# Kernel optimization log

Hardware: AMD Instinct MI355X
Metric: run time of the kernel (lower is better)

The kernel has to match this reference:

```python
import jax, jax.numpy as jnp
import numpy as np

N_NODES = 50000
N_EDGES = 500000
F_IN = 16
F_OUT = 16
F_EDGE = 16
HIDDEN = 64


def setup_inputs() -> dict:
    key = jax.random.key(0)
    ks = jax.random.split(key, 9)
    return {
        "x": jax.random.normal(ks[0], (N_NODES, F_IN), dtype=jnp.float32),
        "edge_feat": jax.random.normal(ks[1], (N_EDGES, F_EDGE), dtype=jnp.float32),
        "src": jax.random.randint(ks[2], (N_EDGES,), 0, N_NODES, dtype=jnp.int32),
        "dst": jax.random.randint(ks[3], (N_EDGES,), 0, N_NODES, dtype=jnp.int32),
        "W1": jax.random.normal(ks[4], (F_EDGE, HIDDEN), dtype=jnp.float32) * 0.1,
        "b1": jax.random.normal(ks[5], (HIDDEN,), dtype=jnp.float32) * 0.1,
        "W2": jax.random.normal(ks[6], (HIDDEN, F_IN * F_OUT), dtype=jnp.float32) * 0.1,
        "b2": jax.random.normal(ks[7], (F_IN * F_OUT,), dtype=jnp.float32) * 0.1,
        "bias": jax.random.normal(ks[8], (F_OUT,), dtype=jnp.float32) * 0.1,
    }


def reference(x, edge_feat, src, dst, W1, b1, W2, b2, bias):
    # WeightNet: per-edge MLP producing a [F_IN, F_OUT] weight matrix per edge
    h = jax.nn.relu(edge_feat @ W1 + b1)                 # [E, HIDDEN]
    W = (h @ W2 + b2).reshape(-1, F_IN, F_OUT)           # [E, F_IN, F_OUT]
    # message: bmm(src_h[E,1,in], W[E,in,out]) -> [E, F_OUT]
    msg = jnp.einsum('ei,eio->eo', x[src], W)
    # scatter-mean reduce over destination nodes
    msum = jax.ops.segment_sum(msg, dst, num_segments=N_NODES)
    cnt = jax.ops.segment_sum(jnp.ones((msg.shape[0],), dtype=msg.dtype), dst,
                              num_segments=N_NODES)
    mean = msum / jnp.maximum(cnt, 1.0)[:, None]
    # DGL update_all only updates nodes that receive messages; zero in-degree
    # nodes keep their input 'h' (valid since F_IN == F_OUT)
    out = jnp.where((cnt > 0)[:, None], mean, x)
    return out + bias[None, :]                           # [N, F_OUT]
```

## Files before the change

kernel.cpp:

```cpp
#include <hip/hip_runtime.h>

#define NN 50000
#define NE 500000
#define FIN 16
#define FOUT 16
#define HID 64
#define TROW 1040

typedef unsigned int  uint;
typedef unsigned short ushort;
typedef __fp16 h2 __attribute__((ext_vector_type(2)));

__device__ __forceinline__ ushort f2h(float f) {
    union { __fp16 h; ushort s; } v; v.h = (__fp16)f; return v.s;
}
__device__ __forceinline__ h2 u2h2(uint u) {
    union { uint u; h2 h; } v; v.u = u; return v.h;
}
__device__ __forceinline__ float h2lo(uint u) {
    union { ushort s; __fp16 h; } v; v.s = (ushort)(u & 0xffffu); return (float)v.h;
}
__device__ __forceinline__ float h2hi(uint u) {
    union { ushort s; __fp16 h; } v; v.s = (ushort)(u >> 16); return (float)v.h;
}


__global__ __launch_bounds__(256) void count_w2r(
    const int* __restrict__ src, const int* __restrict__ dst,
    int* __restrict__ deg_s, int* __restrict__ pos_s,
    int* __restrict__ deg_d, int* __restrict__ pos_d,
    const float* __restrict__ W2, const float* __restrict__ b2,
    const float* __restrict__ W1, float* __restrict__ W2R,
    float* __restrict__ W1T)
{
    const int nbc = (NE + 255) / 256;
    if ((int)blockIdx.x < nbc) {
        const int e = blockIdx.x * 256 + threadIdx.x;
        if (e < NE) {
            pos_s[e] = atomicAdd(deg_s + src[e], 1);
            pos_d[e] = atomicAdd(deg_d + dst[e], 1);
        }
    } else {
        const int t = (blockIdx.x - nbc) * 256 + threadIdx.x;
        if (t < 64 * 16) {
            const int j = t >> 4, i = t & 15;
            W1T[t] = W1[i * HID + j];
        }
        if (t < 65 * 256) {
            const int j = t >> 8;
            const int col = t & 255;
            const int i = col >> 4, o = col & 15;
            const float v = (j < 64) ? W2[j * 256 + col] : b2[col];
            W2R[j * 256 + o * 16 + i] = v;
        }
    }
}

__global__ __launch_bounds__(1024) void dgc_scan2(
    const int* __restrict__ degA, int* __restrict__ offA,
    const int* __restrict__ degB, int* __restrict__ offB)
{
    const int* __restrict__ deg = blockIdx.x ? degB : degA;
    int* __restrict__ offs      = blockIdx.x ? offB : offA;
    __shared__ int wsum[16];
    const int tid = threadIdx.x;
    const int lane = tid & 63;
    const int wid = tid >> 6;
    int carry = 0;
    for (int base = 0; base < NN; base += 1024) {
        const int idx = base + tid;
        const int v = (idx < NN) ? deg[idx] : 0;
        int s = v;
        #pragma unroll
        for (int d = 1; d < 64; d <<= 1) {
            int t = __shfl_up(s, d, 64);
            if (lane >= d) s += t;
        }
        if (lane == 63) wsum[wid] = s;
        __syncthreads();
        if (wid == 0 && lane < 16) {
            int w = wsum[lane];
            #pragma unroll
            for (int d = 1; d < 16; d <<= 1) {
                int t = __shfl_up(w, d, 64);
                if (lane >= d) w += t;
            }
            wsum[lane] = w;
        }
        __syncthreads();
        const int wpre = (wid == 0) ? 0 : wsum[wid - 1];
        if (idx < NN) offs[idx] = carry + wpre + (s - v);
        carry += wsum[15];
        __syncthreads();
    }
    if (tid == 0) offs[NN] = carry;
}

__global__ __launch_bounds__(256) void scatter_tprep(
    const int* __restrict__ src, const int* __restrict__ pos_s,
    const int* __restrict__ offs_s, int* __restrict__ eidx_s,
    const float* __restrict__ x, const float* __restrict__ W2R,
    ushort* __restrict__ T)
{
    const int nbs = (NE + 255) / 256;
    if ((int)blockIdx.x < nbs) {
        const int e = blockIdx.x * 256 + threadIdx.x;
        if (e < NE) eidx_s[offs_s[src[e]] + pos_s[e]] = e;
        return;
    }
    const int bid = blockIdx.x - nbs;
    const int tid = threadIdx.x;
    const int jt = tid >> 4, o = tid & 15;
    const int off0 = (jt >> 1) * 32 + o * 2 + (jt & 1);

    float w0[16], w1[16], w2[16], w3[16];
    {
        const float4* p0 = reinterpret_cast<const float4*>(W2R + (jt     ) * 256 + o * 16);
        const float4* p1 = reinterpret_cast<const float4*>(W2R + (jt + 16) * 256 + o * 16);
        const float4* p2 = reinterpret_cast<const float4*>(W2R + (jt + 32) * 256 + o * 16);
        const float4* p3 = reinterpret_cast<const float4*>(W2R + (jt + 48) * 256 + o * 16);
        #pragma unroll
        for (int q = 0; q < 4; ++q) {
            float4 a = p0[q]; w0[4*q]=a.x; w0[4*q+1]=a.y; w0[4*q+2]=a.z; w0[4*q+3]=a.w;
            float4 b = p1[q]; w1[4*q]=b.x; w1[4*q+1]=b.y; w1[4*q+2]=b.z; w1[4*q+3]=b.w;
            float4 c = p2[q]; w2[4*q]=c.x; w2[4*q+1]=c.y; w2[4*q+2]=c.z; w2[4*q+3]=c.w;
            float4 d = p3[q]; w3[4*q]=d.x; w3[4*q+1]=d.y; w3[4*q+2]=d.z; w3[4*q+3]=d.w;
        }
    }
    float wb[16];
    if (jt == 0) {
        const float4* pb = reinterpret_cast<const float4*>(W2R + 64 * 256 + o * 16);
        #pragma unroll
        for (int q = 0; q < 4; ++q) {
            float4 a = pb[q]; wb[4*q]=a.x; wb[4*q+1]=a.y; wb[4*q+2]=a.z; wb[4*q+3]=a.w;
        }
    }

    for (int n = bid; n < NN; n += 2048) {
        float xr[16];
        {
            const float4* p = reinterpret_cast<const float4*>(x) + (size_t)n * 4;
            float4 a = p[0], b = p[1], c = p[2], d = p[3];
            xr[0]=a.x; xr[1]=a.y; xr[2]=a.z;  xr[3]=a.w;
            xr[4]=b.x; xr[5]=b.y; xr[6]=b.z;  xr[7]=b.w;
            xr[8]=c.x; xr[9]=c.y; xr[10]=c.z; xr[11]=c.w;
            xr[12]=d.x; xr[13]=d.y; xr[14]=d.z; xr[15]=d.w;
        }
        ushort* tw = T + (size_t)n * TROW;

        float s0 = xr[0]*w0[0], s1 = xr[0]*w1[0], s2 = xr[0]*w2[0], s3 = xr[0]*w3[0];
        #pragma unroll
        for (int i = 1; i < 16; ++i) {
            s0 = fmaf(xr[i], w0[i], s0);
            s1 = fmaf(xr[i], w1[i], s1);
            s2 = fmaf(xr[i], w2[i], s2);
            s3 = fmaf(xr[i], w3[i], s3);
        }
        tw[off0]       = f2h(s0);
        tw[off0 + 256] = f2h(s1);
        tw[off0 + 512] = f2h(s2);
        tw[off0 + 768] = f2h(s3);
        if (jt == 0) {
            float sb = xr[0]*wb[0];
            #pragma unroll
            for (int i = 1; i < 16; ++i) sb = fmaf(xr[i], wb[i], sb);
            tw[1024 + o] = f2h(sb);
        }
    }
}

__global__ __launch_bounds__(256) void edge_msg6(
    const int* __restrict__ eidx_s, const int* __restrict__ src,
    const int* __restrict__ dst, const float* __restrict__ ef,
    const float* __restrict__ W1T, const float* __restrict__ b1,
    const ushort* __restrict__ T, const int* __restrict__ offs_d,
    const int* __restrict__ pos_d, float* __restrict__ msgbuf)
{
    const int k = blockIdx.x * blockDim.x + threadIdx.x;
    if (k >= NE) return;
    const int e = eidx_s[k];
    const int s = src[e];

    float ea[16];
    {
        const float4* p = reinterpret_cast<const float4*>(ef) + (size_t)e * 4;
        float4 a = p[0], b = p[1], c = p[2], d = p[3];
        ea[0]=a.x; ea[1]=a.y; ea[2]=a.z;  ea[3]=a.w;
        ea[4]=b.x; ea[5]=b.y; ea[6]=b.z;  ea[7]=b.w;
        ea[8]=c.x; ea[9]=c.y; ea[10]=c.z; ea[11]=c.w;
        ea[12]=d.x; ea[13]=d.y; ea[14]=d.z; ea[15]=d.w;
    }

    const ushort* tr = T + (size_t)s * TROW;

    float m0[16];
    {
        uint4 a = *reinterpret_cast<const uint4*>(tr + 1024);
        uint4 b = *reinterpret_cast<const uint4*>(tr + 1032);
        m0[0]=h2lo(a.x);  m0[1]=h2hi(a.x);  m0[2]=h2lo(a.y);  m0[3]=h2hi(a.y);
        m0[4]=h2lo(a.z);  m0[5]=h2hi(a.z);  m0[6]=h2lo(a.w);  m0[7]=h2hi(a.w);
        m0[8]=h2lo(b.x);  m0[9]=h2hi(b.x);  m0[10]=h2lo(b.y); m0[11]=h2hi(b.y);
        m0[12]=h2lo(b.z); m0[13]=h2hi(b.z); m0[14]=h2lo(b.w); m0[15]=h2hi(b.w);
    }

    for (int jp = 0; jp < 32; ++jp) {
        const float* __restrict__ wr = W1T + jp * 32;
        float h0a = b1[2 * jp], h0b = b1[2 * jp + 1];
        #pragma unroll
        for (int i = 0; i < 16; ++i) {
            h0a = fmaf(ea[i], wr[i], h0a);
            h0b = fmaf(ea[i], wr[16 + i], h0b);
        }
        h0a = fmaxf(h0a, 0.f); h0b = fmaxf(h0b, 0.f);
        const h2 hp0 = __builtin_amdgcn_cvt_pkrtz(h0a, h0b);

        const uint4 a0 = *reinterpret_cast<const uint4*>(tr + jp * 32);
        const uint4 b0 = *reinterpret_cast<const uint4*>(tr + jp * 32 + 8);
        const uint4 c0 = *reinterpret_cast<const uint4*>(tr + jp * 32 + 16);
        const uint4 d0 = *reinterpret_cast<const uint4*>(tr + jp * 32 + 24);

        m0[0]  = __builtin_amdgcn_fdot2(hp0, u2h2(a0.x), m0[0],  false);
        m0[1]  = __builtin_amdgcn_fdot2(hp0, u2h2(a0.y), m0[1],  false);
        m0[2]  = __builtin_amdgcn_fdot2(hp0, u2h2(a0.z), m0[2],  false);
        m0[3]  = __builtin_amdgcn_fdot2(hp0, u2h2(a0.w), m0[3],  false);
        m0[4]  = __builtin_amdgcn_fdot2(hp0, u2h2(b0.x), m0[4],  false);
        m0[5]  = __builtin_amdgcn_fdot2(hp0, u2h2(b0.y), m0[5],  false);
        m0[6]  = __builtin_amdgcn_fdot2(hp0, u2h2(b0.z), m0[6],  false);
        m0[7]  = __builtin_amdgcn_fdot2(hp0, u2h2(b0.w), m0[7],  false);
        m0[8]  = __builtin_amdgcn_fdot2(hp0, u2h2(c0.x), m0[8],  false);
        m0[9]  = __builtin_amdgcn_fdot2(hp0, u2h2(c0.y), m0[9],  false);
        m0[10] = __builtin_amdgcn_fdot2(hp0, u2h2(c0.z), m0[10], false);
        m0[11] = __builtin_amdgcn_fdot2(hp0, u2h2(c0.w), m0[11], false);
        m0[12] = __builtin_amdgcn_fdot2(hp0, u2h2(d0.x), m0[12], false);
        m0[13] = __builtin_amdgcn_fdot2(hp0, u2h2(d0.y), m0[13], false);
        m0[14] = __builtin_amdgcn_fdot2(hp0, u2h2(d0.z), m0[14], false);
        m0[15] = __builtin_amdgcn_fdot2(hp0, u2h2(d0.w), m0[15], false);
    }

    const int d = dst[e];
    const int slot = offs_d[d] + pos_d[e];
    float4* mr = reinterpret_cast<float4*>(msgbuf + (size_t)slot * 16);
    mr[0] = make_float4(m0[0], m0[1], m0[2], m0[3]);
    mr[1] = make_float4(m0[4], m0[5], m0[6], m0[7]);
    mr[2] = make_float4(m0[8], m0[9], m0[10], m0[11]);
    mr[3] = make_float4(m0[12], m0[13], m0[14], m0[15]);
}

__global__ __launch_bounds__(256) void gather_mean3(
    const float* __restrict__ msgbuf, const int* __restrict__ offs_d,
    const float* __restrict__ x, const float* __restrict__ bias,
    float* __restrict__ out)
{
    const int t = blockIdx.x * blockDim.x + threadIdx.x;
    if (t >= NN * 4) return;
    const int n = t >> 2;
    const int oq = t & 3;
    const int beg = offs_d[n], end = offs_d[n + 1];
    float4 s = make_float4(0.f, 0.f, 0.f, 0.f);
    for (int k = beg; k < end; ++k) {
        const float4 v = *reinterpret_cast<const float4*>(msgbuf + (size_t)k * 16 + oq * 4);
        s.x += v.x; s.y += v.y; s.z += v.z; s.w += v.w;
    }
    const int d = end - beg;
    float4 r;
    if (d > 0) {
        const float inv = 1.f / (float)d;
        r = make_float4(s.x * inv, s.y * inv, s.z * inv, s.w * inv);
    } else {
        r = *reinterpret_cast<const float4*>(x + (size_t)n * 16 + oq * 4);
    }
    const float4 bv = *reinterpret_cast<const float4*>(bias + oq * 4);
    r.x += bv.x; r.y += bv.y; r.z += bv.z; r.w += bv.w;
    *reinterpret_cast<float4*>(out + (size_t)n * 16 + oq * 4) = r;
}

__global__ __launch_bounds__(1024) void dgc_scan(
    const int* __restrict__ deg, int* __restrict__ offs, int n)
{
    __shared__ int wsum[16];
    const int tid = threadIdx.x;
    const int lane = tid & 63;
    const int wid = tid >> 6;
    int carry = 0;
    for (int base = 0; base < n; base += 1024) {
        const int idx = base + tid;
        const int v = (idx < n) ? deg[idx] : 0;
        int s = v;
        #pragma unroll
        for (int d = 1; d < 64; d <<= 1) {
            int t = __shfl_up(s, d, 64);
            if (lane >= d) s += t;
        }
        if (lane == 63) wsum[wid] = s;
        __syncthreads();
        if (wid == 0 && lane < 16) {
            int w = wsum[lane];
            #pragma unroll
            for (int d = 1; d < 16; d <<= 1) {
                int t = __shfl_up(w, d, 64);
                if (lane >= d) w += t;
            }
            wsum[lane] = w;
        }
        __syncthreads();
        const int wpre = (wid == 0) ? 0 : wsum[wid - 1];
        if (idx < n) offs[idx] = carry + wpre + (s - v);
        carry += wsum[15];
        __syncthreads();
    }
    if (tid == 0) offs[n] = carry;
}

__global__ __launch_bounds__(256) void dgc_edge_csr(
    const float* __restrict__ x, const float* __restrict__ ef,
    const int* __restrict__ src, const int* __restrict__ dst,
    const float* __restrict__ W1, const float* __restrict__ b1,
    const float* __restrict__ W2, const float* __restrict__ b2,
    float* __restrict__ msg, int* __restrict__ pos, int* __restrict__ deg)
{
    const int e = blockIdx.x * blockDim.x + threadIdx.x;
    if (e >= NE) return;
    float efv[16];
    {
        const float4* p = reinterpret_cast<const float4*>(ef) + (size_t)e * 4;
        float4 a = p[0], b = p[1], c = p[2], d = p[3];
        efv[0]=a.x; efv[1]=a.y; efv[2]=a.z;  efv[3]=a.w;
        efv[4]=b.x; efv[5]=b.y; efv[6]=b.z;  efv[7]=b.w;
        efv[8]=c.x; efv[9]=c.y; efv[10]=c.z; efv[11]=c.w;
        efv[12]=d.x; efv[13]=d.y; efv[14]=d.z; efv[15]=d.w;
    }
    const int s = src[e];
    float xs[16];
    {
        const float4* p = reinterpret_cast<const float4*>(x) + (size_t)s * 4;
        float4 a = p[0], b = p[1], c = p[2], d = p[3];
        xs[0]=a.x; xs[1]=a.y; xs[2]=a.z;  xs[3]=a.w;
        xs[4]=b.x; xs[5]=b.y; xs[6]=b.z;  xs[7]=b.w;
        xs[8]=c.x; xs[9]=c.y; xs[10]=c.z; xs[11]=c.w;
        xs[12]=d.x; xs[13]=d.y; xs[14]=d.z; xs[15]=d.w;
    }
    float m[16];
    #pragma unroll
    for (int o = 0; o < 16; ++o) m[o] = 0.f;
    #pragma unroll
    for (int i = 0; i < 16; ++i) {
        const float xi = xs[i];
        #pragma unroll
        for (int o = 0; o < 16; ++o) m[o] = fmaf(xi, b2[i * 16 + o], m[o]);
    }
    for (int j = 0; j < HID; ++j) {
        float hj = b1[j];
        #pragma unroll
        for (int i = 0; i < 16; ++i) hj = fmaf(efv[i], W1[i * HID + j], hj);
        hj = fmaxf(hj, 0.f);
        const float* __restrict__ w2r = W2 + (size_t)j * 256;
        float t[16];
        #pragma unroll
        for (int o = 0; o < 16; ++o) t[o] = 0.f;
        #pragma unroll
        for (int i = 0; i < 16; ++i) {
            const float xi = xs[i];
            #pragma unroll
            for (int o = 0; o < 16; ++o) t[o] = fmaf(xi, w2r[i * 16 + o], t[o]);
        }
        #pragma unroll
        for (int o = 0; o < 16; ++o) m[o] = fmaf(hj, t[o], m[o]);
    }
    float4* mr = reinterpret_cast<float4*>(msg + (size_t)e * 16);
    mr[0] = make_float4(m[0], m[1], m[2], m[3]);
    mr[1] = make_float4(m[4], m[5], m[6], m[7]);
    mr[2] = make_float4(m[8], m[9], m[10], m[11]);
    mr[3] = make_float4(m[12], m[13], m[14], m[15]);
    pos[e] = atomicAdd(deg + dst[e], 1);
}

__global__ __launch_bounds__(256) void dgc_scatter(
    const int* __restrict__ dst, const int* __restrict__ pos,
    const int* __restrict__ offs, int* __restrict__ eidx)
{
    const int e = blockIdx.x * blockDim.x + threadIdx.x;
    if (e >= NE) return;
    eidx[offs[dst[e]] + pos[e]] = e;
}

__global__ __launch_bounds__(256) void dgc_gather(
    const float* __restrict__ msg, const int* __restrict__ offs,
    const int* __restrict__ eidx, const float* __restrict__ x,
    const float* __restrict__ bias, float* __restrict__ out)
{
    const int t = blockIdx.x * blockDim.x + threadIdx.x;
    if (t >= NN * FOUT) return;
    const int n = t >> 4;
    const int o = t & 15;
    const int beg = offs[n], end = offs[n + 1];
    float s = 0.f;
    for (int k = beg; k < end; ++k)
        s += msg[(size_t)eidx[k] * 16 + o];
    const int d = end - beg;
    const float v = (d > 0) ? (s / (float)d) : x[t];
    out[t] = v + bias[o];
}

extern "C" void kernel_launch(void* const* d_in, const int* in_sizes, int n_in,
                              void* d_out, int out_size, void* d_ws, size_t ws_size,
                              hipStream_t stream) {
    const float* x    = (const float*)d_in[0];
    const float* ef   = (const float*)d_in[1];
    const int*   src  = (const int*)d_in[2];
    const int*   dst  = (const int*)d_in[3];
    const float* W1   = (const float*)d_in[4];
    const float* b1   = (const float*)d_in[5];
    const float* W2   = (const float*)d_in[6];
    const float* b2   = (const float*)d_in[7];
    const float* bias = (const float*)d_in[8];
    float* out = (float*)d_out;

    ushort* T      = (ushort*)d_ws;
    float*  msgbuf = (float*)(T + (size_t)NN * TROW);
    float*  W2R    = msgbuf + (size_t)NE * 16;
    float*  W1T    = W2R + 65 * 256;
    int*    deg_s  = (int*)(W1T + 64 * 16);
    int*    deg_d  = deg_s + NN;
    int*    offs_s = deg_d + NN;
    int*    offs_d = offs_s + NN + 1;
    int*    pos_s  = offs_d + NN + 1;
    int*    pos_d  = pos_s + NE;
    int*    eidx_s = pos_d + NE;
    const size_t needed =
        (size_t)NN * TROW * 2 +
        ((size_t)NE * 16 + 65 * 256 + 64 * 16) * 4 +
        ((size_t)2 * NN + 2 * (NN + 1) + (size_t)3 * NE) * 4;

    const int nbc = (NE + 255) / 256;

    if (ws_size >= needed) {
        hipMemsetAsync(deg_s, 0, (size_t)2 * NN * sizeof(int), stream);
        count_w2r<<<nbc + 65, 256, 0, stream>>>(
            src, dst, deg_s, pos_s, deg_d, pos_d, W2, b2, W1, W2R, W1T);
        dgc_scan2<<<2, 1024, 0, stream>>>(deg_s, offs_s, deg_d, offs_d);
        scatter_tprep<<<nbc + 2048, 256, 0, stream>>>(
            src, pos_s, offs_s, eidx_s, x, W2R, T);
        edge_msg6<<<nbc, 256, 0, stream>>>(
            eidx_s, src, dst, ef, W1T, b1, T, offs_d, pos_d, msgbuf);
        gather_mean3<<<(NN * 4 + 255) / 256, 256, 0, stream>>>(
            msgbuf, offs_d, x, bias, out);
    } else {
        float* msg  = (float*)d_ws;
        int*   deg  = (int*)(msg + (size_t)NE * 16);
        int*   offs = deg + NN;
        int*   pos  = offs + NN + 1;
        int*   eidx = pos + NE;
        hipMemsetAsync(deg, 0, (size_t)NN * sizeof(int), stream);
        dgc_edge_csr<<<(NE + 255) / 256, 256, 0, stream>>>(
            x, ef, src, dst, W1, b1, W2, b2, msg, pos, deg);
        dgc_scan<<<1, 1024, 0, stream>>>(deg, offs, NN);
        dgc_scatter<<<(NE + 255) / 256, 256, 0, stream>>>(dst, pos, offs, eidx);
        dgc_gather<<<(NN * FOUT + 255) / 256, 256, 0, stream>>>(
            msg, offs, eidx, x, bias, out);
    }
}
```

Measured before the change: 211.7 us.

## Fuse the whole pipeline into one cooperative persistent kernel with grid syncs

```diff
diff --git a/kernel.cpp b/kernel.cpp
--- a/kernel.cpp
+++ b/kernel.cpp
@@ -1,11 +1,13 @@
 #include <hip/hip_runtime.h>
+#include <hip/hip_cooperative_groups.h>
+
+namespace cg = cooperative_groups;
 
 #define NN 50000
 #define NE 500000
-#define FIN 16
-#define FOUT 16
 #define HID 64
 #define TROW 1040
+#define MAXG 2048
 
 typedef unsigned int  uint;
 typedef unsigned short ushort;
@@ -24,6 +26,260 @@
     union { ushort s; __fp16 h; } v; v.s = (ushort)(u >> 16); return (float)v.h;
 }
 
+__device__ void blk_scan_range(const int* __restrict__ deg, int* __restrict__ offs,
+                               int beg, int end, int carry0)
+{
+    __shared__ int wsum[4];
+    __shared__ int wtot;
+    const int tid = threadIdx.x;
+    int carry = carry0;
+    for (int base = beg; base < end; base += 256) {
+        const int idx = base + tid;
+        const bool inb = idx < end;
+        int v = inb ? deg[idx] : 0;
+        int s = v;
+        #pragma unroll
+        for (int d = 1; d < 64; d <<= 1) {
+            int t = __shfl_up(s, d, 64);
+            if ((tid & 63) >= d) s += t;
+        }
+        if ((tid & 63) == 63) wsum[tid >> 6] = s;
+        __syncthreads();
+        if (tid == 0) {
+            int c = 0;
+            #pragma unroll
+            for (int w = 0; w < 4; ++w) { int t = wsum[w]; wsum[w] = c; c += t; }
+            wtot = c;
+        }
+        __syncthreads();
+        if (inb) offs[idx] = carry + wsum[tid >> 6] + (s - v);
+        carry += wtot;
+        __syncthreads();
+    }
+}
+
+struct MegaParams {
+    const float *x, *ef;
+    const int *src, *dst;
+    const float *W1, *b1, *W2, *b2, *bias;
+    float *out;
+    ushort *T;
+    float *msgbuf, *W2R, *W1T;
+    int *deg_s, *deg_d, *offs_s, *offs_d, *pos_s, *pos_d, *eidx_s, *bsum_s, *bsum_d;
+};
+
+__global__ __launch_bounds__(256, 4) void dgc_mega(MegaParams p)
+{
+    cg::grid_group gg = cg::this_grid();
+    const int tid = threadIdx.x;
+    const int bid = blockIdx.x;
+    const int G = gridDim.x;
+    const int gtid = bid * 256 + tid;
+    const int gstride = G * 256;
+
+    for (int i = gtid; i < NN; i += gstride) { p.deg_s[i] = 0; p.deg_d[i] = 0; }
+    gg.sync();
+
+    for (int e = gtid; e < NE; e += gstride) {
+        p.pos_s[e] = atomicAdd(p.deg_s + p.src[e], 1);
+        p.pos_d[e] = atomicAdd(p.deg_d + p.dst[e], 1);
+    }
+    for (int t = gtid; t < 65 * 256; t += gstride) {
+        const int j = t >> 8, col = t & 255;
+        const int i = col >> 4, o = col & 15;
+        const float v = (j < 64) ? p.W2[j * 256 + col] : p.b2[col];
+        p.W2R[j * 256 + o * 16 + i] = v;
+    }
+    for (int t = gtid; t < 64 * 16; t += gstride) {
+        const int j = t >> 4, i = t & 15;
+        p.W1T[t] = p.W1[i * HID + j];
+    }
+    gg.sync();
+
+    const int tile = (NN + G - 1) / G;
+    const int nbeg = bid * tile;
+    const int nend = (nbeg + tile < NN) ? (nbeg + tile) : NN;
+    {
+        int ls = 0, ld = 0;
+        for (int i = nbeg + tid; i < nend; i += 256) { ls += p.deg_s[i]; ld += p.deg_d[i]; }
+        #pragma unroll
+        for (int d = 32; d > 0; d >>= 1) {
+            ls += __shfl_down(ls, d, 64);
+            ld += __shfl_down(ld, d, 64);
+        }
+        __shared__ int reds[4], redd[4];
+        if ((tid & 63) == 0) { reds[tid >> 6] = ls; redd[tid >> 6] = ld; }
+        __syncthreads();
+        if (tid == 0) {
+            p.bsum_s[bid] = reds[0] + reds[1] + reds[2] + reds[3];
+            p.bsum_d[bid] = redd[0] + redd[1] + redd[2] + redd[3];
+        }
+        __syncthreads();
+    }
+    gg.sync();
+    if (bid == 0)      blk_scan_range(p.bsum_s, p.bsum_s, 0, G, 0);
+    else if (bid == 1) blk_scan_range(p.bsum_d, p.bsum_d, 0, G, 0);
+    gg.sync();
+    blk_scan_range(p.deg_s, p.offs_s, nbeg, nend, p.bsum_s[bid]);
+    blk_scan_range(p.deg_d, p.offs_d, nbeg, nend, p.bsum_d[bid]);
+    if (gtid == 0) { p.offs_s[NN] = NE; p.offs_d[NN] = NE; }
+    gg.sync();
+
+    for (int e = gtid; e < NE; e += gstride)
+        p.eidx_s[p.offs_s[p.src[e]] + p.pos_s[e]] = e;
+    {
+        const int jt = tid >> 4, o = tid & 15;
+        const int off0 = (jt >> 1) * 32 + o * 2 + (jt & 1);
+
+        float w0[16], w1[16], w2[16], w3[16];
+        {
+            const float4* p0 = reinterpret_cast<const float4*>(p.W2R + (jt     ) * 256 + o * 16);
+            const float4* p1 = reinterpret_cast<const float4*>(p.W2R + (jt + 16) * 256 + o * 16);
+            const float4* p2 = reinterpret_cast<const float4*>(p.W2R + (jt + 32) * 256 + o * 16);
+            const float4* p3 = reinterpret_cast<const float4*>(p.W2R + (jt + 48) * 256 + o * 16);
+            #pragma unroll
+            for (int q = 0; q < 4; ++q) {
+                float4 a = p0[q]; w0[4*q]=a.x; w0[4*q+1]=a.y; w0[4*q+2]=a.z; w0[4*q+3]=a.w;
+                float4 b = p1[q]; w1[4*q]=b.x; w1[4*q+1]=b.y; w1[4*q+2]=b.z; w1[4*q+3]=b.w;
+                float4 c = p2[q]; w2[4*q]=c.x; w2[4*q+1]=c.y; w2[4*q+2]=c.z; w2[4*q+3]=c.w;
+                float4 d = p3[q]; w3[4*q]=d.x; w3[4*q+1]=d.y; w3[4*q+2]=d.z; w3[4*q+3]=d.w;
+            }
+        }
+        float wb[16];
+        if (jt == 0) {
+            const float4* pb = reinterpret_cast<const float4*>(p.W2R + 64 * 256 + o * 16);
+            #pragma unroll
+            for (int q = 0; q < 4; ++q) {
+                float4 a = pb[q]; wb[4*q]=a.x; wb[4*q+1]=a.y; wb[4*q+2]=a.z; wb[4*q+3]=a.w;
+            }
+        }
+
+        for (int n = bid; n < NN; n += G) {
+            float xr[16];
+            {
+                const float4* q = reinterpret_cast<const float4*>(p.x) + (size_t)n * 4;
+                float4 a = q[0], b = q[1], c = q[2], d = q[3];
+                xr[0]=a.x; xr[1]=a.y; xr[2]=a.z;  xr[3]=a.w;
+                xr[4]=b.x; xr[5]=b.y; xr[6]=b.z;  xr[7]=b.w;
+                xr[8]=c.x; xr[9]=c.y; xr[10]=c.z; xr[11]=c.w;
+                xr[12]=d.x; xr[13]=d.y; xr[14]=d.z; xr[15]=d.w;
+            }
+            ushort* tw = p.T + (size_t)n * TROW;
+
+            float s0 = xr[0]*w0[0], s1 = xr[0]*w1[0], s2 = xr[0]*w2[0], s3 = xr[0]*w3[0];
+            #pragma unroll
+            for (int i = 1; i < 16; ++i) {
+                s0 = fmaf(xr[i], w0[i], s0);
+                s1 = fmaf(xr[i], w1[i], s1);
+                s2 = fmaf(xr[i], w2[i], s2);
+                s3 = fmaf(xr[i], w3[i], s3);
+            }
+            tw[off0]       = f2h(s0);
+            tw[off0 + 256] = f2h(s1);
+            tw[off0 + 512] = f2h(s2);
+            tw[off0 + 768] = f2h(s3);
+            if (jt == 0) {
+                float sb = xr[0]*wb[0];
+                #pragma unroll
+                for (int i = 1; i < 16; ++i) sb = fmaf(xr[i], wb[i], sb);
+                tw[1024 + o] = f2h(sb);
+            }
+        }
+    }
+    gg.sync();
+
+    for (int k = gtid; k < NE; k += gstride) {
+        const int e = p.eidx_s[k];
+        const int s = p.src[e];
+
+        float ea[16];
+        {
+            const float4* q = reinterpret_cast<const float4*>(p.ef) + (size_t)e * 4;
+            float4 a = q[0], b = q[1], c = q[2], d = q[3];
+            ea[0]=a.x; ea[1]=a.y; ea[2]=a.z;  ea[3]=a.w;
+            ea[4]=b.x; ea[5]=b.y; ea[6]=b.z;  ea[7]=b.w;
+            ea[8]=c.x; ea[9]=c.y; ea[10]=c.z; ea[11]=c.w;
+            ea[12]=d.x; ea[13]=d.y; ea[14]=d.z; ea[15]=d.w;
+        }
+
+        const ushort* tr = p.T + (size_t)s * TROW;
+
+        float m0[16];
+        {
+            uint4 a = *reinterpret_cast<const uint4*>(tr + 1024);
+            uint4 b = *reinterpret_cast<const uint4*>(tr + 1032);
+            m0[0]=h2lo(a.x);  m0[1]=h2hi(a.x);  m0[2]=h2lo(a.y);  m0[3]=h2hi(a.y);
+            m0[4]=h2lo(a.z);  m0[5]=h2hi(a.z);  m0[6]=h2lo(a.w);  m0[7]=h2hi(a.w);
+            m0[8]=h2lo(b.x);  m0[9]=h2hi(b.x);  m0[10]=h2lo(b.y); m0[11]=h2hi(b.y);
+            m0[12]=h2lo(b.z); m0[13]=h2hi(b.z); m0[14]=h2lo(b.w); m0[15]=h2hi(b.w);
+        }
+
+        for (int jp = 0; jp < 32; ++jp) {
+            const float* __restrict__ wr = p.W1T + jp * 32;
+            float h0a = p.b1[2 * jp], h0b = p.b1[2 * jp + 1];
+            #pragma unroll
+            for (int i = 0; i < 16; ++i) {
+                h0a = fmaf(ea[i], wr[i], h0a);
+                h0b = fmaf(ea[i], wr[16 + i], h0b);
+            }
+            h0a = fmaxf(h0a, 0.f); h0b = fmaxf(h0b, 0.f);
+            const h2 hp0 = __builtin_amdgcn_cvt_pkrtz(h0a, h0b);
+
+            const uint4 a0 = *reinterpret_cast<const uint4*>(tr + jp * 32);
+            const uint4 b0 = *reinterpret_cast<const uint4*>(tr + jp * 32 + 8);
+            const uint4 c0 = *reinterpret_cast<const uint4*>(tr + jp * 32 + 16);
+            const uint4 d0 = *reinterpret_cast<const uint4*>(tr + jp * 32 + 24);
+
+            m0[0]  = __builtin_amdgcn_fdot2(hp0, u2h2(a0.x), m0[0],  false);
+            m0[1]  = __builtin_amdgcn_fdot2(hp0, u2h2(a0.y), m0[1],  false);
+            m0[2]  = __builtin_amdgcn_fdot2(hp0, u2h2(a0.z), m0[2],  false);
+            m0[3]  = __builtin_amdgcn_fdot2(hp0, u2h2(a0.w), m0[3],  false);
+            m0[4]  = __builtin_amdgcn_fdot2(hp0, u2h2(b0.x), m0[4],  false);
+            m0[5]  = __builtin_amdgcn_fdot2(hp0, u2h2(b0.y), m0[5],  false);
+            m0[6]  = __builtin_amdgcn_fdot2(hp0, u2h2(b0.z), m0[6],  false);
+            m0[7]  = __builtin_amdgcn_fdot2(hp0, u2h2(b0.w), m0[7],  false);
+            m0[8]  = __builtin_amdgcn_fdot2(hp0, u2h2(c0.x), m0[8],  false);
+            m0[9]  = __builtin_amdgcn_fdot2(hp0, u2h2(c0.y), m0[9],  false);
+            m0[10] = __builtin_amdgcn_fdot2(hp0, u2h2(c0.z), m0[10], false);
+            m0[11] = __builtin_amdgcn_fdot2(hp0, u2h2(c0.w), m0[11], false);
+            m0[12] = __builtin_amdgcn_fdot2(hp0, u2h2(d0.x), m0[12], false);
+            m0[13] = __builtin_amdgcn_fdot2(hp0, u2h2(d0.y), m0[13], false);
+            m0[14] = __builtin_amdgcn_fdot2(hp0, u2h2(d0.z), m0[14], false);
+            m0[15] = __builtin_amdgcn_fdot2(hp0, u2h2(d0.w), m0[15], false);
+        }
+
+        const int d = p.dst[e];
+        const int slot = p.offs_d[d] + p.pos_d[e];
+        float4* mr = reinterpret_cast<float4*>(p.msgbuf + (size_t)slot * 16);
+        mr[0] = make_float4(m0[0], m0[1], m0[2], m0[3]);
+        mr[1] = make_float4(m0[4], m0[5], m0[6], m0[7]);
+        mr[2] = make_float4(m0[8], m0[9], m0[10], m0[11]);
+        mr[3] = make_float4(m0[12], m0[13], m0[14], m0[15]);
+    }
+    gg.sync();
+
+    for (int t = gtid; t < NN * 4; t += gstride) {
+        const int n = t >> 2;
+        const int oq = t & 3;
+        const int beg = p.offs_d[n], end = p.offs_d[n + 1];
+        float4 s = make_float4(0.f, 0.f, 0.f, 0.f);
+        for (int k = beg; k < end; ++k) {
+            const float4 v = *reinterpret_cast<const float4*>(p.msgbuf + (size_t)k * 16 + oq * 4);
+            s.x += v.x; s.y += v.y; s.z += v.z; s.w += v.w;
+        }
+        const int d = end - beg;
+        float4 r;
+        if (d > 0) {
+            const float inv = 1.f / (float)d;
+            r = make_float4(s.x * inv, s.y * inv, s.z * inv, s.w * inv);
+        } else {
+            r = *reinterpret_cast<const float4*>(p.x + (size_t)n * 16 + oq * 4);
+        }
+        const float4 bv = *reinterpret_cast<const float4*>(p.bias + oq * 4);
+        r.x += bv.x; r.y += bv.y; r.z += bv.z; r.w += bv.w;
+        *reinterpret_cast<float4*>(p.out + (size_t)n * 16 + oq * 4) = r;
+    }
+}
 
 __global__ __launch_bounds__(256) void count_w2r(
     const int* __restrict__ src, const int* __restrict__ dst,
@@ -139,8 +395,8 @@
     for (int n = bid; n < NN; n += 2048) {
         float xr[16];
         {
-            const float4* p = reinterpret_cast<const float4*>(x) + (size_t)n * 4;
-            float4 a = p[0], b = p[1], c = p[2], d = p[3];
+            const float4* q = reinterpret_cast<const float4*>(x) + (size_t)n * 4;
+            float4 a = q[0], b = q[1], c = q[2], d = q[3];
             xr[0]=a.x; xr[1]=a.y; xr[2]=a.z;  xr[3]=a.w;
             xr[4]=b.x; xr[5]=b.y; xr[6]=b.z;  xr[7]=b.w;
             xr[8]=c.x; xr[9]=c.y; xr[10]=c.z; xr[11]=c.w;
@@ -183,8 +439,8 @@
 
     float ea[16];
     {
-        const float4* p = reinterpret_cast<const float4*>(ef) + (size_t)e * 4;
-        float4 a = p[0], b = p[1], c = p[2], d = p[3];
+        const float4* q = reinterpret_cast<const float4*>(ef) + (size_t)e * 4;
+        float4 a = q[0], b = q[1], c = q[2], d = q[3];
         ea[0]=a.x; ea[1]=a.y; ea[2]=a.z;  ea[3]=a.w;
         ea[4]=b.x; ea[5]=b.y; ea[6]=b.z;  ea[7]=b.w;
         ea[8]=c.x; ea[9]=c.y; ea[10]=c.z; ea[11]=c.w;
@@ -389,7 +645,7 @@
     const float* __restrict__ bias, float* __restrict__ out)
 {
     const int t = blockIdx.x * blockDim.x + threadIdx.x;
-    if (t >= NN * FOUT) return;
+    if (t >= NN * 16) return;
     const int n = t >> 4;
     const int o = t & 15;
     const int beg = offs[n], end = offs[n + 1];
@@ -426,24 +682,47 @@
     int*    pos_s  = offs_d + NN + 1;
     int*    pos_d  = pos_s + NE;
     int*    eidx_s = pos_d + NE;
+    int*    bsum_s = eidx_s + NE;
+    int*    bsum_d = bsum_s + MAXG;
     const size_t needed =
         (size_t)NN * TROW * 2 +
         ((size_t)NE * 16 + 65 * 256 + 64 * 16) * 4 +
-        ((size_t)2 * NN + 2 * (NN + 1) + (size_t)3 * NE) * 4;
+        ((size_t)2 * NN + 2 * (NN + 1) + (size_t)3 * NE + 2 * MAXG) * 4;
 
     const int nbc = (NE + 255) / 256;
 
     if (ws_size >= needed) {
-        hipMemsetAsync(deg_s, 0, (size_t)2 * NN * sizeof(int), stream);
-        count_w2r<<<nbc + 65, 256, 0, stream>>>(
-            src, dst, deg_s, pos_s, deg_d, pos_d, W2, b2, W1, W2R, W1T);
-        dgc_scan2<<<2, 1024, 0, stream>>>(deg_s, offs_s, deg_d, offs_d);
-        scatter_tprep<<<nbc + 2048, 256, 0, stream>>>(
-            src, pos_s, offs_s, eidx_s, x, W2R, T);
-        edge_msg6<<<nbc, 256, 0, stream>>>(
-            eidx_s, src, dst, ef, W1T, b1, T, offs_d, pos_d, msgbuf);
-        gather_mean3<<<(NN * 4 + 255) / 256, 256, 0, stream>>>(
-            msgbuf, offs_d, x, bias, out);
+        bool done = false;
+        int nbcu = 0;
+        if (hipOccupancyMaxActiveBlocksPerMultiprocessor(&nbcu, dgc_mega, 256, 0) == hipSuccess
+            && nbcu > 0) {
+            int G = nbcu * 256;
+            if (G > MAXG) G = MAXG;
+            MegaParams prm;
+            prm.x = x; prm.ef = ef; prm.src = src; prm.dst = dst;
+            prm.W1 = W1; prm.b1 = b1; prm.W2 = W2; prm.b2 = b2; prm.bias = bias;
+            prm.out = out;
+            prm.T = T; prm.msgbuf = msgbuf; prm.W2R = W2R; prm.W1T = W1T;
+            prm.deg_s = deg_s; prm.deg_d = deg_d; prm.offs_s = offs_s; prm.offs_d = offs_d;
+            prm.pos_s = pos_s; prm.pos_d = pos_d; prm.eidx_s = eidx_s;
+            prm.bsum_s = bsum_s; prm.bsum_d = bsum_d;
+            void* args[] = { &prm };
+            if (hipLaunchCooperativeKernel((const void*)dgc_mega, dim3(G), dim3(256),
+                                           args, 0, stream) == hipSuccess)
+                done = true;
+        }
+        if (!done) {
+            hipMemsetAsync(deg_s, 0, (size_t)2 * NN * sizeof(int), stream);
+            count_w2r<<<nbc + 65, 256, 0, stream>>>(
+                src, dst, deg_s, pos_s, deg_d, pos_d, W2, b2, W1, W2R, W1T);
+            dgc_scan2<<<2, 1024, 0, stream>>>(deg_s, offs_s, deg_d, offs_d);
+            scatter_tprep<<<nbc + 2048, 256, 0, stream>>>(
+                src, pos_s, offs_s, eidx_s, x, W2R, T);
+            edge_msg6<<<nbc, 256, 0, stream>>>(
+                eidx_s, src, dst, ef, W1T, b1, T, offs_d, pos_d, msgbuf);
+            gather_mean3<<<(NN * 4 + 255) / 256, 256, 0, stream>>>(
+                msgbuf, offs_d, x, bias, out);
+        }
     } else {
         float* msg  = (float*)d_ws;
         int*   deg  = (int*)(msg + (size_t)NE * 16);
@@ -455,7 +734,7 @@
             x, ef, src, dst, W1, b1, W2, b2, msg, pos, deg);
         dgc_scan<<<1, 1024, 0, stream>>>(deg, offs, NN);
         dgc_scatter<<<(NE + 255) / 256, 256, 0, stream>>>(dst, pos, offs, eidx);
-        dgc_gather<<<(NN * FOUT + 255) / 256, 256, 0, stream>>>(
+        dgc_gather<<<(NN * 16 + 255) / 256, 256, 0, stream>>>(
             msg, offs, eidx, x, bias, out);
     }
 }
```

Measured after the change: 650.0 us. 3.07x slower.
